# Kernel optimization log

Measured on AMD Instinct MI355X. Metric: run time of the kernel, lower is better.

## Reference

```python
import math
import jax, jax.numpy as jnp
import numpy as np

B, T, D = 4, 1024, 1024
H = 16
HD = D // H       # head_dim
DE = 64           # d_event
NT = 8            # n_event_types
NR = 64           # n_rules
NH = 4            # n_hits
NA = 2            # n_alternatives
SQ = math.sqrt(HD)


def setup_inputs() -> dict:
    key = jax.random.key(0)
    ks = jax.random.split(key, 16)
    s = 0.02
    f = jnp.float32
    return {
        "x": jax.random.normal(ks[0], (B, T, D), f),
        "W_node": jax.random.normal(ks[1], (D, D), f) * s,
        "W_value": jax.random.normal(ks[2], (D, D), f) * s,
        "W_out": jax.random.normal(ks[3], (D, D), f) * s,
        "arity_w": jax.random.normal(ks[4], (H, HD), f) * s,   # arity=3 -> one extra axis weight
        "W_event": jax.random.normal(ks[5], (D, DE), f) * s,
        "W_type": jax.random.normal(ks[6], (D, NT), f) * s,
        "patterns": jax.random.normal(ks[7], (NR, DE), f) * s,
        "W_actions": jax.random.normal(ks[8], (NA, D, D), f) * s,
        "W_alt": jax.random.normal(ks[9], (DE, NA), f) * s,
        "log_temp": jnp.zeros((), f),
        "Wg1": jax.random.normal(ks[10], (2 * D + 1, D), f) * s,
        "bg1": jnp.zeros((D,), f),
        "Wg2": jax.random.normal(ks[11], (D, 1), f) * s,
        "bg2": jnp.zeros((1,), f),
    }


def reference(x, W_node, W_value, W_out, arity_w, W_event, W_type, patterns,
              W_actions, W_alt, log_temp, Wg1, bg1, Wg2, bg2):
    # --- IsotropicAttention (arity=3, eval mode so dropout is identity) ---
    nodes = (x @ W_node).reshape(B, T, H, HD).transpose(0, 2, 1, 3)    # (B,H,T,HD)
    values = (x @ W_value).reshape(B, T, H, HD).transpose(0, 2, 1, 3)  # (B,H,T,HD)
    scores = jnp.einsum('bhtd,bhsd->bhts', nodes, nodes)
    scores = (scores + scores.transpose(0, 1, 3, 2)) * (0.5 / SQ)      # symmetrize + scale
    ax = jnp.einsum('bhtd,hd->bht', nodes, arity_w)                    # ternary axis score
    mod = jax.nn.sigmoid((ax[:, :, :, None] + ax[:, :, None, :]) / SQ)
    scores = scores * mod
    attn = jax.nn.softmax(scores, axis=-1)
    attn_out = jnp.einsum('bhts,bhsd->bthd', attn, values).reshape(B, T, D) @ W_out
    x1 = x + attn_out
    # --- EventGenerator ---
    events = x1 @ W_event                                              # (B,T,DE)
    event_types = jax.nn.softmax(x1 @ W_type, axis=-1)                 # (B,T,NT)
    # --- RuleBank: soft top-k hit activation ---
    en = events / jnp.maximum(jnp.linalg.norm(events, axis=-1, keepdims=True), 1e-12)
    pn = patterns / jnp.maximum(jnp.linalg.norm(patterns, axis=-1, keepdims=True), 1e-12)
    sim = en @ pn.T                                                    # (B,T,NR)
    topk_vals, topk_idx = jax.lax.top_k(sim, NH)
    temp = jnp.clip(jnp.exp(log_temp), 0.01, 10.0)
    hit_w = jax.nn.softmax(topk_vals / temp, axis=-1)                  # (B,T,NH)
    hit_patterns = patterns[topk_idx]                                  # (B,T,NH,DE)
    weighted_pattern = jnp.einsum('btkd,btk->btd', hit_patterns, hit_w)
    alt_w = jax.nn.softmax((weighted_pattern @ W_alt) / temp, axis=-1) # (B,T,NA)
    acted = jnp.einsum('btd,ade->btae', x1, W_actions)                 # (B,T,NA,D)
    actions_out = jnp.einsum('btae,bta->bte', acted, alt_w)
    hit_strength = jnp.max(topk_vals, axis=-1, keepdims=True)
    actions_out = actions_out * jax.nn.sigmoid(hit_strength)
    # --- TransactionGate: soft commit/rollback ---
    entropy = -jnp.sum(event_types * jnp.log(event_types + 1e-10), axis=-1, keepdims=True)
    entropy_norm = entropy / math.log(NT)
    gin = jnp.concatenate([x1, actions_out, entropy_norm], axis=-1)    # (B,T,2D+1)
    g = jax.nn.sigmoid(jax.nn.silu(gin @ Wg1 + bg1) @ Wg2 + bg2)       # (B,T,1)
    return x1 + g * actions_out
```

## Files before the change

### kernel.cpp

```cpp
#include <hip/hip_runtime.h>
#include <hip/hip_bf16.h>
#include <math.h>

#define B_  4
#define T_  1024
#define D_  1024
#define H_  16
#define HD_ 64
#define DE_ 64
#define NT_ 8
#define NR_ 64
#define NH_ 4

typedef __attribute__((ext_vector_type(8))) short short8;
typedef __attribute__((ext_vector_type(4))) short short4v;
typedef __attribute__((ext_vector_type(2))) unsigned uint2v;
typedef __attribute__((ext_vector_type(4))) float f4;

__device__ __forceinline__ short f2bf(float f) {
    unsigned x = __float_as_uint(f);
    unsigned r = (x + 0x7fffu + ((x >> 16) & 1u)) >> 16;
    return (short)r;
}
__device__ __forceinline__ float bf2f(short s) {
    return __uint_as_float(((unsigned)(unsigned short)s) << 16);
}

__device__ __forceinline__ int swz64(int row, int slot) {
    return row * 64 + ((slot ^ (row & 7)) << 3);
}

struct TJ { const float* src; short* dst; int K, N, rs, ro, base; };
struct TJobs { TJ j[7]; };

__global__ __launch_bounds__(256) void prep_k(
    const float* __restrict__ x, short* __restrict__ xb, TJobs jb,
    const float* __restrict__ Wt, short* __restrict__ BTe,
    const float* __restrict__ patterns, float* __restrict__ pn)
{
    const int bid = blockIdx.x;
    const int tid = threadIdx.x;
    __shared__ float tile[64][65];

    if (bid < 2048) {
        size_t i = ((size_t)bid * 256 + tid) * 8;
        float4 v0 = *(const float4*)&x[i];
        float4 v1 = *(const float4*)&x[i + 4];
        short8 o;
        o[0] = f2bf(v0.x); o[1] = f2bf(v0.y); o[2] = f2bf(v0.z); o[3] = f2bf(v0.w);
        o[4] = f2bf(v1.x); o[5] = f2bf(v1.y); o[6] = f2bf(v1.z); o[7] = f2bf(v1.w);
        *(short8*)&xb[i] = o;
        return;
    }
    if (bid < 3856) {
        int ji = 0;
#pragma unroll
        for (int i = 1; i < 7; i++) if (bid >= jb.j[i].base) ji = i;
        const float* src = jb.j[ji].src;
        short* dst = jb.j[ji].dst;
        const int K = jb.j[ji].K, N = jb.j[ji].N;
        const int rs = jb.j[ji].rs, ro = jb.j[ji].ro;
        int rel = bid - jb.j[ji].base;
        int tiles_n = N >> 6;
        int k0 = (rel / tiles_n) * 64, n0 = (rel % tiles_n) * 64;
        const int r = tid >> 4, c = (tid & 15) * 4;
#pragma unroll
        for (int rep = 0; rep < 4; rep++) {
            int rr = rep * 16 + r;
            float4 v = *(const float4*)&src[(size_t)(k0 + rr) * N + n0 + c];
            tile[rr][c] = v.x; tile[rr][c + 1] = v.y; tile[rr][c + 2] = v.z; tile[rr][c + 3] = v.w;
        }
        __syncthreads();
#pragma unroll
        for (int rep = 0; rep < 4; rep++) {
            int n = rep * 16 + r;
            short4v p;
            p[0] = f2bf(tile[c + 0][n]);
            p[1] = f2bf(tile[c + 1][n]);
            p[2] = f2bf(tile[c + 2][n]);
            p[3] = f2bf(tile[c + 3][n]);
            *(short4v*)&dst[(size_t)((n0 + n) * rs + ro) * K + k0 + c] = p;
        }
        return;
    }
    if (bid < 3888) {
        int idx = (bid - 3856) * 256 + tid;
        int n = idx >> 10, k = idx & 1023;
        BTe[(size_t)(64 + n) * 1024 + k] = f2bf(Wt[k * 8 + n]);
        return;
    }
    {
        int r = (bid - 3888) * 4 + (tid >> 6);
        int lane = tid & 63;
        float v = patterns[r * 64 + lane];
        float ss = v * v;
        for (int off = 1; off < 64; off <<= 1) ss += __shfl_xor(ss, off);
        pn[r * 64 + lane] = v / fmaxf(sqrtf(ss), 1e-12f);
    }
}

template<int AM>
__global__ __launch_bounds__(256) void gemm8(
    const short* __restrict__ A1, const short* __restrict__ A2, int Ks,
    const short* __restrict__ BT,
    float* __restrict__ C, short* __restrict__ Cb1, short* __restrict__ Cb2,
    int M, int N, int K, int epi,
    const float* __restrict__ resid, const float* __restrict__ ent,
    const float* __restrict__ w1e, const float* __restrict__ bias,
    const float* __restrict__ altw, const float* __restrict__ hitsig)
{
    constexpr int BM = AM * 32;
    constexpr int AR = (AM == 4) ? 2 : 4;
    constexpr int ANV = 64 / AR / 8;
    __shared__ short As[BM * 72];
    __shared__ short Bs[64 * 72];
    const int tid = threadIdx.x, wave = tid >> 6, lane = tid & 63;
    const int lrow = lane & 15, lq = lane >> 4;
    int bid = blockIdx.x;
    int tiles_m = M / BM;
    int mpx = tiles_m >> 3;
    int xcd = bid & 7, idx = bid >> 3;
    int mt = xcd * mpx + (idx % mpx);
    int nt = idx / mpx;
    const int m0 = mt * BM, n0 = nt * 64;
    const int wm = (wave >> 1) * (AM * 16), wn = (wave & 1) * 32;
    const int K2 = K - Ks;
    const int arow = tid / AR, ash = (tid % AR) * (64 / AR);
    const int brow = tid >> 2, bsh = (tid & 3) * 16;

    short8 va[ANV], vb[2];
    auto loadA = [&](int k0) {
        int ka = k0 + ash;
        const short* ap = (ka < Ks)
            ? A1 + (size_t)(m0 + arow) * Ks + ka
            : A2 + (size_t)(m0 + arow) * K2 + (ka - Ks);
#pragma unroll
        for (int u = 0; u < ANV; u++) va[u] = *(const short8*)(ap + u * 8);
    };
    auto loadB = [&](int k0) {
        const short* bp = BT + (size_t)(n0 + brow) * K + k0 + bsh;
#pragma unroll
        for (int u = 0; u < 2; u++) vb[u] = *(const short8*)(bp + u * 8);
    };

    loadA(0); loadB(0);
    f4 acc[AM][2] = {};

    for (int k0 = 0; k0 < K; k0 += 64) {
        __syncthreads();
#pragma unroll
        for (int u = 0; u < ANV; u++)
            *(short8*)&As[arow * 72 + ash + u * 8] = va[u];
#pragma unroll
        for (int u = 0; u < 2; u++)
            *(short8*)&Bs[brow * 72 + bsh + u * 8] = vb[u];
        __syncthreads();
        if (k0 + 64 < K) { loadA(k0 + 64); loadB(k0 + 64); }
        __builtin_amdgcn_sched_barrier(0);
#pragma unroll
        for (int kh = 0; kh < 2; kh++) {
            short8 af[AM], bfv[2];
#pragma unroll
            for (int i = 0; i < AM; i++)
                af[i] = *(short8*)&As[(wm + i * 16 + lrow) * 72 + kh * 32 + lq * 8];
#pragma unroll
            for (int j = 0; j < 2; j++)
                bfv[j] = *(short8*)&Bs[(wn + j * 16 + lrow) * 72 + kh * 32 + lq * 8];
#pragma unroll
            for (int i = 0; i < AM; i++)
#pragma unroll
                for (int j = 0; j < 2; j++)
                    acc[i][j] = __builtin_amdgcn_mfma_f32_16x16x32_bf16(
                        af[i], bfv[j], acc[i][j], 0, 0, 0);
        }
    }

    if (epi == 3) {
#pragma unroll
        for (int i = 0; i < AM; i++) {
#pragma unroll
            for (int r = 0; r < 4; r++) {
                int row = m0 + wm + i * 16 + lq * 4 + r;
                float gp = 0.f;
#pragma unroll
                for (int j = 0; j < 2; j++) {
                    int col = n0 + wn + j * 16 + lrow;
                    float v = acc[i][j][r] + ent[row] * w1e[col] + bias[col];
                    float sv = v * __builtin_amdgcn_rcpf(1.f + __expf(-v));
                    gp += sv * altw[col];
                }
                gp += __shfl_xor(gp, 1);
                gp += __shfl_xor(gp, 2);
                gp += __shfl_xor(gp, 4);
                gp += __shfl_xor(gp, 8);
                if (lrow == 0) atomicAdd(&C[row], gp);
            }
        }
        return;
    }

#pragma unroll
    for (int i = 0; i < AM; i++) {
#pragma unroll
        for (int r = 0; r < 4; r++) {
            int row = m0 + wm + i * 16 + lq * 4 + r;
            float w0 = 0.f, w1 = 0.f, hs = 0.f;
            if (epi == 5) { w0 = altw[row * 2]; w1 = altw[row * 2 + 1]; hs = hitsig[row]; }
#pragma unroll
            for (int j = 0; j < 2; j++) {
                int col = n0 + wn + j * 16 + lrow;
                float v = acc[i][j][r];
                if (epi == 0) {
                    C[(size_t)row * N + col] = v;
                } else if (epi == 1) {
                    v += resid[(size_t)row * N + col];
                    C[(size_t)row * N + col] = v;
                    Cb1[(size_t)row * N + col] = f2bf(v);
                } else if (epi == 2) {
                    if (col < 1024) Cb1[(size_t)row * 1024 + col] = f2bf(v);
                    else            Cb2[(size_t)row * 1024 + col - 1024] = f2bf(v);
                } else {
                    float other = __shfl_xor(v, 1);
                    if ((lane & 1) == 0) {
                        float cv = (w0 * v + w1 * other) * hs;
                        Cb1[(size_t)row * 1024 + (col >> 1)] = f2bf(cv);
                    }
                }
            }
        }
    }
}

__global__ __launch_bounds__(256) void vx_k(
    const short* __restrict__ vb, short* __restrict__ vtg,
    const short* __restrict__ nodes_bf, const float* __restrict__ arity_w,
    float* __restrict__ ax)
{
    const int bid = blockIdx.x;
    const int tid = threadIdx.x;
    __shared__ short tile[64 * 72];

    if (bid < 1024) {
        const int b = bid >> 8, h = (bid >> 4) & 15, t0 = (bid & 15) * 64;
        const int row = tid >> 2, c = (tid & 3) * 16;
        const short* p = vb + (size_t)(b * T_ + t0 + row) * D_ + h * 64 + c;
        *(short8*)&tile[row * 72 + c + 0] = *(const short8*)(p + 0);
        *(short8*)&tile[row * 72 + c + 8] = *(const short8*)(p + 8);
        __syncthreads();
        short8 o0, o1;
#pragma unroll
        for (int i = 0; i < 8; i++) o0[i] = tile[(c + i) * 72 + row];
#pragma unroll
        for (int i = 0; i < 8; i++) o1[i] = tile[(c + 8 + i) * 72 + row];
        short* q = vtg + (size_t)((b * H_ + h) * 64 + row) * T_ + t0 + c;
        *(short8*)(q + 0) = o0;
        *(short8*)(q + 8) = o1;
        return;
    }
    {
        int idx = (bid - 1024) * 256 + tid;
        int t = idx & (T_ - 1);
        int h = (idx >> 10) & (H_ - 1);
        int b = idx >> 14;
        const short* np_ = nodes_bf + (((size_t)b * T_ + t) * H_ + h) * HD_;
        float s = 0.f;
#pragma unroll
        for (int d = 0; d < HD_; d += 8) {
            short8 n8 = *(const short8*)&np_[d];
#pragma unroll
            for (int q = 0; q < 8; q++) s += bf2f(n8[q]) * arity_w[h * HD_ + d + q];
        }
        ax[idx] = s;
    }
}

__global__ __launch_bounds__(256) void attn9_k(
    const short* __restrict__ nodes_bf, const short* __restrict__ vtg,
    const float* __restrict__ ax, short* __restrict__ attnp)
{
    const int b = blockIdx.z, h = blockIdx.y, t0 = blockIdx.x * 64;
    const int tid = threadIdx.x;
    const int wave = tid >> 6, lane = tid & 63;
    const int lrow = lane & 15, lq = lane >> 4;
    const int wm = wave * 16;
    const int row = tid >> 2, c4 = tid & 3;

    __shared__ short Ns[2][64 * 64];
    __shared__ short Vt[2][64 * 64];
    __shared__ short Pm[64 * 64];

    const short* qp = nodes_bf + (size_t)(b * T_ + t0 + wm + lrow) * D_ + h * 64;
    const short8 bt0 = *(const short8*)(qp + lq * 8);
    const short8 bt1 = *(const short8*)(qp + 32 + lq * 8);
    const float at8 = ax[(size_t)(b * H_ + h) * T_ + t0 + wm + lrow] * 0.125f;

    const short* np0 = nodes_bf + (size_t)(b * T_ + row) * D_ + h * 64 + c4 * 16;
    const short* vp0 = vtg + (size_t)((b * H_ + h) * 64 + row) * T_ + c4 * 16;
    const float* axp_ = ax + (size_t)(b * H_ + h) * T_;

    short8 vn0, vn1, vv0, vv1;
    f4 axv[4];
    auto preload = [&](int s0) {
        const short* np = np0 + (size_t)s0 * D_;
        const short* vp = vp0 + s0;
        vn0 = *(const short8*)(np + 0);
        vn1 = *(const short8*)(np + 8);
        vv0 = *(const short8*)(vp + 0);
        vv1 = *(const short8*)(vp + 8);
#pragma unroll
        for (int j = 0; j < 4; j++)
            axv[j] = *(const f4*)&axp_[s0 + j * 16 + lq * 4];
    };

    preload(0);

    float l_reg = 0.f;
    f4 O[4] = {};
    f4 axc[4];

    for (int t = 0; t < T_ / 64; t++) {
        const int cur = t & 1;
        *(short8*)&Ns[cur][swz64(row, 2 * c4 + 0)] = vn0;
        *(short8*)&Ns[cur][swz64(row, 2 * c4 + 1)] = vn1;
        *(short8*)&Vt[cur][swz64(row, 2 * c4 + 0)] = vv0;
        *(short8*)&Vt[cur][swz64(row, 2 * c4 + 1)] = vv1;
#pragma unroll
        for (int j = 0; j < 4; j++) axc[j] = axv[j];
        __syncthreads();
        if (t + 1 < T_ / 64) preload((t + 1) * 64);
        __builtin_amdgcn_sched_barrier(0);

        float psum = 0.f;
#pragma unroll
        for (int j = 0; j < 4; j++) {
            short8 a0 = *(short8*)&Ns[cur][swz64(j * 16 + lrow, lq)];
            short8 a1 = *(short8*)&Ns[cur][swz64(j * 16 + lrow, 4 + lq)];
            f4 s = {0.f, 0.f, 0.f, 0.f};
            __builtin_amdgcn_s_setprio(1);
            s = __builtin_amdgcn_mfma_f32_16x16x32_bf16(a0, bt0, s, 0, 0, 0);
            s = __builtin_amdgcn_mfma_f32_16x16x32_bf16(a1, bt1, s, 0, 0, 0);
            __builtin_amdgcn_s_setprio(0);
            float p0, p1, p2, p3;
            {
                float z, zz, t1, mK;
                z = fmaf(axc[j][0], 0.125f, at8); zz = z * z;
                t1 = fmaf(zz, -0.0037570183f, 0.04508422f);
                mK = fmaf(z, t1, 0.09016844f);
                p0 = __builtin_amdgcn_exp2f(s[0] * mK);
                z = fmaf(axc[j][1], 0.125f, at8); zz = z * z;
                t1 = fmaf(zz, -0.0037570183f, 0.04508422f);
                mK = fmaf(z, t1, 0.09016844f);
                p1 = __builtin_amdgcn_exp2f(s[1] * mK);
                z = fmaf(axc[j][2], 0.125f, at8); zz = z * z;
                t1 = fmaf(zz, -0.0037570183f, 0.04508422f);
                mK = fmaf(z, t1, 0.09016844f);
                p2 = __builtin_amdgcn_exp2f(s[2] * mK);
                z = fmaf(axc[j][3], 0.125f, at8); zz = z * z;
                t1 = fmaf(zz, -0.0037570183f, 0.04508422f);
                mK = fmaf(z, t1, 0.09016844f);
                p3 = __builtin_amdgcn_exp2f(s[3] * mK);
            }
            psum += (p0 + p1) + (p2 + p3);
            unsigned u0, u1;
            asm("v_cvt_pk_bf16_f32 %0, %1, %2" : "=v"(u0) : "v"(p0), "v"(p1));
            asm("v_cvt_pk_bf16_f32 %0, %1, %2" : "=v"(u1) : "v"(p2), "v"(p3));
            uint2v uu; uu[0] = u0; uu[1] = u1;
            *(uint2v*)&Pm[swz64(wm + lrow, 2 * j + (lq >> 1)) + (lq & 1) * 4] = uu;
        }
        l_reg += psum;

        short8 pa0 = *(short8*)&Pm[swz64(wm + lrow, lq)];
        short8 pa1 = *(short8*)&Pm[swz64(wm + lrow, 4 + lq)];
        __builtin_amdgcn_s_setprio(1);
#pragma unroll
        for (int dj = 0; dj < 4; dj++) {
            short8 v0 = *(short8*)&Vt[cur][swz64(dj * 16 + lrow, lq)];
            short8 v1 = *(short8*)&Vt[cur][swz64(dj * 16 + lrow, 4 + lq)];
            O[dj] = __builtin_amdgcn_mfma_f32_16x16x32_bf16(pa0, v0, O[dj], 0, 0, 0);
            O[dj] = __builtin_amdgcn_mfma_f32_16x16x32_bf16(pa1, v1, O[dj], 0, 0, 0);
        }
        __builtin_amdgcn_s_setprio(0);
    }

    l_reg += __shfl_xor(l_reg, 16);
    l_reg += __shfl_xor(l_reg, 32);

    float linv[4];
#pragma unroll
    for (int r = 0; r < 4; r++)
        linv[r] = __builtin_amdgcn_rcpf(__shfl(l_reg, lq * 4 + r));
#pragma unroll
    for (int dj = 0; dj < 4; dj++)
#pragma unroll
        for (int r = 0; r < 4; r++)
            attnp[(size_t)(b * T_ + t0 + wm + lq * 4 + r) * D_ + h * 64 + dj * 16 + lrow] =
                f2bf(O[dj][r] * linv[r]);
}

__global__ __launch_bounds__(256) void token2_k(
    const float* __restrict__ evlg, const float* __restrict__ pn,
    const float* __restrict__ patterns, const float* __restrict__ W_alt,
    const float* __restrict__ log_temp,
    float* __restrict__ entn, float* __restrict__ altw, float* __restrict__ hitsig,
    float* __restrict__ gsum)
{
    const int tid = threadIdx.x, wave = tid >> 6, lane = tid & 63;
    __shared__ float pn_sh[64 * 68];
    __shared__ float pat_sh[64 * 68];
    __shared__ float en_sh[4][68];
    {
        int row = tid >> 2, c = (tid & 3) * 16;
#pragma unroll
        for (int u = 0; u < 4; u++) {
            *(float4*)&pn_sh[row * 68 + c + u * 4]  = *(const float4*)&pn[row * 64 + c + u * 4];
            *(float4*)&pat_sh[row * 68 + c + u * 4] = *(const float4*)&patterns[row * 64 + c + u * 4];
        }
    }
    float temp = expf(log_temp[0]);
    temp = fminf(fmaxf(temp, 0.01f), 10.f);
    const float tinv = 1.f / temp;
    __syncthreads();

#pragma unroll
    for (int rep = 0; rep < 2; rep++) {
        const int m = blockIdx.x * 8 + wave * 2 + rep;
        float ev = evlg[(size_t)m * 128 + lane];
        float ss = ev * ev;
        for (int off = 1; off < 64; off <<= 1) ss += __shfl_xor(ss, off);
        float en = ev * __builtin_amdgcn_rcpf(fmaxf(sqrtf(ss), 1e-12f));
        en_sh[wave][lane] = en;
        float entv;
        {
            float lgt = evlg[(size_t)m * 128 + 64 + (lane & 7)];
            float mx = lgt;
            for (int off = 1; off < 8; off <<= 1) mx = fmaxf(mx, __shfl_xor(mx, off));
            float p = __expf(lgt - mx);
            float sum = p;
            for (int off = 1; off < 8; off <<= 1) sum += __shfl_xor(sum, off);
            float pi = p / sum;
            float term = -pi * __logf(pi + 1e-10f);
            float e = term;
            for (int off = 1; off < 8; off <<= 1) e += __shfl_xor(e, off);
            entv = e * 0.4808983f;
        }
        float sim = 0.f;
#pragma unroll
        for (int u = 0; u < 16; u++) {
            float4 e4 = *(float4*)&en_sh[wave][u * 4];
            float4 p4 = *(float4*)&pn_sh[lane * 68 + u * 4];
            sim += e4.x * p4.x + e4.y * p4.y + e4.z * p4.z + e4.w * p4.w;
        }
        float v = sim;
        float tv[NH_]; int tix[NH_];
#pragma unroll
        for (int kk = 0; kk < NH_; kk++) {
            float mv = v; int mi = lane;
            if (v == -1e30f) mi = 127;
            for (int off = 1; off < 64; off <<= 1) {
                float ov = __shfl_xor(mv, off);
                int   oi = __shfl_xor(mi, off);
                if (ov > mv || (ov == mv && oi < mi)) { mv = ov; mi = oi; }
            }
            tv[kk] = mv; tix[kk] = mi;
            if (lane == mi) v = -1e30f;
        }
        float hmx = tv[0];
        float hw[NH_], hsum = 0.f;
#pragma unroll
        for (int kk = 0; kk < NH_; kk++) { hw[kk] = __expf((tv[kk] - hmx) * tinv); hsum += hw[kk]; }
        float hsr = __builtin_amdgcn_rcpf(hsum);
        float wp = 0.f;
#pragma unroll
        for (int kk = 0; kk < NH_; kk++) wp += hw[kk] * hsr * pat_sh[tix[kk] * 68 + lane];
        float a0 = wp * W_alt[lane * 2 + 0];
        float a1 = wp * W_alt[lane * 2 + 1];
        for (int off = 1; off < 64; off <<= 1) {
            a0 += __shfl_xor(a0, off);
            a1 += __shfl_xor(a1, off);
        }
        a0 *= tinv; a1 *= tinv;
        float amx = fmaxf(a0, a1);
        float e0 = __expf(a0 - amx), e1 = __expf(a1 - amx);
        if (lane == 0) {
            float zr = __builtin_amdgcn_rcpf(e0 + e1);
            altw[m * 2 + 0] = e0 * zr;
            altw[m * 2 + 1] = e1 * zr;
            hitsig[m] = __builtin_amdgcn_rcpf(1.f + __expf(-tv[0]));
            entn[m] = entv;
            gsum[m] = 0.f;
        }
    }
}

__global__ __launch_bounds__(256) void gate2_k(
    const float* __restrict__ gsum, const float* __restrict__ bg2,
    const float* __restrict__ x1, const short* __restrict__ actions_bf,
    float* __restrict__ out)
{
    const int m = blockIdx.x, tid = threadIdx.x;
    float g = 1.f / (1.f + __expf(-(gsum[m] + bg2[0])));
    size_t i = (size_t)m * D_ + tid * 4;
    float4 xv = *(const float4*)&x1[i];
    short4v av = *(const short4v*)&actions_bf[i];
    float4 o;
    o.x = xv.x + g * bf2f(av[0]);
    o.y = xv.y + g * bf2f(av[1]);
    o.z = xv.z + g * bf2f(av[2]);
    o.w = xv.w + g * bf2f(av[3]);
    *(float4*)&out[i] = o;
}

extern "C" void kernel_launch(void* const* d_in, const int* in_sizes, int n_in,
                              void* d_out, int out_size, void* d_ws, size_t ws_size,
                              hipStream_t stream)
{
    const float* x        = (const float*)d_in[0];
    const float* W_node   = (const float*)d_in[1];
    const float* W_value  = (const float*)d_in[2];
    const float* W_out    = (const float*)d_in[3];
    const float* arity_w  = (const float*)d_in[4];
    const float* W_event  = (const float*)d_in[5];
    const float* W_type   = (const float*)d_in[6];
    const float* patterns = (const float*)d_in[7];
    const float* W_act    = (const float*)d_in[8];
    const float* W_alt    = (const float*)d_in[9];
    const float* log_temp = (const float*)d_in[10];
    const float* Wg1      = (const float*)d_in[11];
    const float* bg1      = (const float*)d_in[12];
    const float* Wg2      = (const float*)d_in[13];
    const float* bg2      = (const float*)d_in[14];
    float* out = (float*)d_out;

    const int M = B_ * T_;
    float* x1     = (float*)d_ws;
    float* evlg   = x1 + 4194304;
    float* axp    = evlg + 524288;
    float* pn     = axp + 65536;
    float* entn   = pn + 4096;
    float* altw   = entn + 4096;
    float* hitsig = altw + 8192;
    float* gsum   = axp;
    short* big       = (short*)(hitsig + 4096);
    short* xbf       = big;
    short* nodes_bf  = big + 1 * 4194304;
    short* values_bf = big + 2 * 4194304;
    short* vtg       = big + 3 * 4194304;
    short* x1_bf     = big + 4 * 4194304;
    short* wts       = big + 5 * 4194304;
    short* WnvT  = wts;
    short* WoT   = wts + 2 * 1048576;
    short* WaT   = wts + 3 * 1048576;
    short* Wg1T  = wts + 5 * 1048576;
    short* BTe   = wts + 7 * 1048576;
    short* actions_bf = vtg;

    dim3 blk(256);
    dim3 g_bh(T_ / 64, H_, B_);

    TJobs jb;
    jb.j[0] = {W_node,            WnvT,           1024, 1024, 1, 0, 2048};
    jb.j[1] = {W_value,           WnvT + 1048576, 1024, 1024, 1, 0, 2304};
    jb.j[2] = {W_out,             WoT,            1024, 1024, 1, 0, 2560};
    jb.j[3] = {W_act,             WaT,            1024, 1024, 2, 0, 2816};
    jb.j[4] = {W_act + 1048576,   WaT,            1024, 1024, 2, 1, 3072};
    jb.j[5] = {Wg1,               Wg1T,           2048, 1024, 1, 0, 3328};
    jb.j[6] = {W_event,           BTe,            1024,   64, 1, 0, 3840};
    prep_k<<<3904, blk, 0, stream>>>(x, xbf, jb, W_type, BTe, patterns, pn);

    gemm8<2><<<2048, blk, 0, stream>>>(xbf, xbf, D_, WnvT,
        nullptr, nodes_bf, values_bf, M, 2048, D_, 2,
        nullptr, nullptr, nullptr, nullptr, nullptr, nullptr);
    vx_k<<<1280, blk, 0, stream>>>(values_bf, vtg, nodes_bf, arity_w, axp);
    attn9_k<<<g_bh, blk, 0, stream>>>(nodes_bf, vtg, axp, xbf);
    gemm8<2><<<1024, blk, 0, stream>>>(xbf, xbf, D_, WoT,
        x1, x1_bf, nullptr, M, D_, D_, 1,
        x, nullptr, nullptr, nullptr, nullptr, nullptr);
    gemm8<2><<<128, blk, 0, stream>>>(x1_bf, x1_bf, D_, BTe,
        evlg, nullptr, nullptr, M, 128, D_, 0,
        nullptr, nullptr, nullptr, nullptr, nullptr, nullptr);
    token2_k<<<M / 8, blk, 0, stream>>>(evlg, pn, patterns, W_alt, log_temp,
                                        entn, altw, hitsig, gsum);
    gemm8<4><<<1024, blk, 0, stream>>>(x1_bf, x1_bf, D_, WaT,
        nullptr, actions_bf, nullptr, M, 2048, D_, 5,
        nullptr, nullptr, nullptr, nullptr, altw, hitsig);
    gemm8<2><<<1024, blk, 0, stream>>>(x1_bf, actions_bf, D_, Wg1T,
        gsum, nullptr, nullptr, M, D_, 2048, 3,
        nullptr, entn, Wg1 + (size_t)2048 * D_, bg1, Wg2, nullptr);
    gate2_k<<<M, blk, 0, stream>>>(gsum, bg2, x1, actions_bf, out);
}
```

Baseline: 316.4 us.

## Stage GEMM tiles via direct global-to-LDS loads with double-buffered swizzled shared memory

Replaces the register-staged GEMM tile loads with global_load_lds direct-to-LDS transfers into two shared-memory buffers. The next K-step's tiles are issued before the MFMAs on the current buffer run, and an XOR swizzle replaces the padded stride to avoid bank conflicts. The action GEMM also moves from a 128-row tile to a 64-row tile with twice the blocks. The cost is doubled LDS use and reliance on the async load being complete when the barrier is reached.

Result: no change. 311.1 us (-1.7%).

```diff
diff --git a/kernel.cpp b/kernel.cpp
--- a/kernel.cpp
+++ b/kernel.cpp
@@ -17,6 +17,9 @@
 typedef __attribute__((ext_vector_type(2))) unsigned uint2v;
 typedef __attribute__((ext_vector_type(4))) float f4;
 
+typedef __attribute__((address_space(1))) const unsigned int guint;
+typedef __attribute__((address_space(3))) unsigned int suint;
+
 __device__ __forceinline__ short f2bf(float f) {
     unsigned x = __float_as_uint(f);
     unsigned r = (x + 0x7fffu + ((x >> 16) & 1u)) >> 16;
@@ -100,7 +103,7 @@
 }
 
 template<int AM>
-__global__ __launch_bounds__(256) void gemm8(
+__global__ __launch_bounds__(256) void gemm11(
     const short* __restrict__ A1, const short* __restrict__ A2, int Ks,
     const short* __restrict__ BT,
     float* __restrict__ C, short* __restrict__ Cb1, short* __restrict__ Cb2,
@@ -110,10 +113,9 @@
     const float* __restrict__ altw, const float* __restrict__ hitsig)
 {
     constexpr int BM = AM * 32;
-    constexpr int AR = (AM == 4) ? 2 : 4;
-    constexpr int ANV = 64 / AR / 8;
-    __shared__ short As[BM * 72];
-    __shared__ short Bs[64 * 72];
+    constexpr int AISS = BM / 32;
+    __shared__ short As[2][BM * 64];
+    __shared__ short Bs[2][64 * 64];
     const int tid = threadIdx.x, wave = tid >> 6, lane = tid & 63;
     const int lrow = lane & 15, lq = lane >> 4;
     int bid = blockIdx.x;
@@ -125,47 +127,53 @@
     const int m0 = mt * BM, n0 = nt * 64;
     const int wm = (wave >> 1) * (AM * 16), wn = (wave & 1) * 32;
     const int K2 = K - Ks;
-    const int arow = tid / AR, ash = (tid % AR) * (64 / AR);
-    const int brow = tid >> 2, bsh = (tid & 3) * 16;
-
-    short8 va[ANV], vb[2];
-    auto loadA = [&](int k0) {
-        int ka = k0 + ash;
-        const short* ap = (ka < Ks)
-            ? A1 + (size_t)(m0 + arow) * Ks + ka
-            : A2 + (size_t)(m0 + arow) * K2 + (ka - Ks);
-#pragma unroll
-        for (int u = 0; u < ANV; u++) va[u] = *(const short8*)(ap + u * 8);
+
+    const int l8 = lane >> 3;
+    const int cs = ((lane & 7) ^ l8) << 3;
+
+    auto stageA = [&](int k0, int bu) {
+#pragma unroll
+        for (int u = 0; u < AISS; u++) {
+            int r = wave * (AISS * 8) + u * 8 + l8;
+            int ka = k0 + cs;
+            const short* gp = (ka < Ks)
+                ? A1 + (size_t)(m0 + r) * Ks + ka
+                : A2 + (size_t)(m0 + r) * K2 + (ka - Ks);
+            short* lp = &As[bu][wave * (AISS * 512) + u * 512];
+            __builtin_amdgcn_global_load_lds((guint*)gp, (suint*)lp, 16, 0, 0);
+        }
     };
-    auto loadB = [&](int k0) {
-        const short* bp = BT + (size_t)(n0 + brow) * K + k0 + bsh;
-#pragma unroll
-        for (int u = 0; u < 2; u++) vb[u] = *(const short8*)(bp + u * 8);
+    auto stageB = [&](int k0, int bu) {
+#pragma unroll
+        for (int u = 0; u < 2; u++) {
+            int r = wave * 16 + u * 8 + l8;
+            const short* gp = BT + (size_t)(n0 + r) * K + k0 + cs;
+            short* lp = &Bs[bu][wave * 1024 + u * 512];
+            __builtin_amdgcn_global_load_lds((guint*)gp, (suint*)lp, 16, 0, 0);
+        }
     };
 
-    loadA(0); loadB(0);
+    stageA(0, 0); stageB(0, 0);
+    __syncthreads();
     f4 acc[AM][2] = {};
-
-    for (int k0 = 0; k0 < K; k0 += 64) {
-        __syncthreads();
-#pragma unroll
-        for (int u = 0; u < ANV; u++)
-            *(short8*)&As[arow * 72 + ash + u * 8] = va[u];
-#pragma unroll
-        for (int u = 0; u < 2; u++)
-            *(short8*)&Bs[brow * 72 + bsh + u * 8] = vb[u];
-        __syncthreads();
-        if (k0 + 64 < K) { loadA(k0 + 64); loadB(k0 + 64); }
+    const int nsteps = K >> 6;
+    int cur = 0;
+
+    for (int t = 0; t < nsteps; t++) {
+        if (t + 1 < nsteps) {
+            stageA((t + 1) << 6, cur ^ 1);
+            stageB((t + 1) << 6, cur ^ 1);
+        }
         __builtin_amdgcn_sched_barrier(0);
 #pragma unroll
         for (int kh = 0; kh < 2; kh++) {
             short8 af[AM], bfv[2];
 #pragma unroll
             for (int i = 0; i < AM; i++)
-                af[i] = *(short8*)&As[(wm + i * 16 + lrow) * 72 + kh * 32 + lq * 8];
+                af[i] = *(short8*)&As[cur][swz64(wm + i * 16 + lrow, kh * 4 + lq)];
 #pragma unroll
             for (int j = 0; j < 2; j++)
-                bfv[j] = *(short8*)&Bs[(wn + j * 16 + lrow) * 72 + kh * 32 + lq * 8];
+                bfv[j] = *(short8*)&Bs[cur][swz64(wn + j * 16 + lrow, kh * 4 + lq)];
 #pragma unroll
             for (int i = 0; i < AM; i++)
 #pragma unroll
@@ -173,6 +181,8 @@
                     acc[i][j] = __builtin_amdgcn_mfma_f32_16x16x32_bf16(
                         af[i], bfv[j], acc[i][j], 0, 0, 0);
         }
+        __syncthreads();
+        cur ^= 1;
     }
 
     if (epi == 3) {
@@ -567,23 +577,23 @@
     jb.j[6] = {W_event,           BTe,            1024,   64, 1, 0, 3840};
     prep_k<<<3904, blk, 0, stream>>>(x, xbf, jb, W_type, BTe, patterns, pn);
 
-    gemm8<2><<<2048, blk, 0, stream>>>(xbf, xbf, D_, WnvT,
+    gemm11<2><<<2048, blk, 0, stream>>>(xbf, xbf, D_, WnvT,
         nullptr, nodes_bf, values_bf, M, 2048, D_, 2,
         nullptr, nullptr, nullptr, nullptr, nullptr, nullptr);
     vx_k<<<1280, blk, 0, stream>>>(values_bf, vtg, nodes_bf, arity_w, axp);
     attn9_k<<<g_bh, blk, 0, stream>>>(nodes_bf, vtg, axp, xbf);
-    gemm8<2><<<1024, blk, 0, stream>>>(xbf, xbf, D_, WoT,
+    gemm11<2><<<1024, blk, 0, stream>>>(xbf, xbf, D_, WoT,
         x1, x1_bf, nullptr, M, D_, D_, 1,
         x, nullptr, nullptr, nullptr, nullptr, nullptr);
-    gemm8<2><<<128, blk, 0, stream>>>(x1_bf, x1_bf, D_, BTe,
+    gemm11<2><<<128, blk, 0, stream>>>(x1_bf, x1_bf, D_, BTe,
         evlg, nullptr, nullptr, M, 128, D_, 0,
         nullptr, nullptr, nullptr, nullptr, nullptr, nullptr);
     token2_k<<<M / 8, blk, 0, stream>>>(evlg, pn, patterns, W_alt, log_temp,
                                         entn, altw, hitsig, gsum);
-    gemm8<4><<<1024, blk, 0, stream>>>(x1_bf, x1_bf, D_, WaT,
+    gemm11<2><<<2048, blk, 0, stream>>>(x1_bf, x1_bf, D_, WaT,
         nullptr, actions_bf, nullptr, M, 2048, D_, 5,
         nullptr, nullptr, nullptr, nullptr, altw, hitsig);
-    gemm8<2><<<1024, blk, 0, stream>>>(x1_bf, actions_bf, D_, Wg1T,
+    gemm11<2><<<1024, blk, 0, stream>>>(x1_bf, actions_bf, D_, Wg1T,
         gsum, nullptr, nullptr, M, D_, 2048, 3,
         nullptr, entn, Wg1 + (size_t)2048 * D_, bg1, Wg2, nullptr);
     gate2_k<<<M, blk, 0, stream>>>(gsum, bg2, x1, actions_bf, out);
```
